# Kernel tuning notes

Hardware: AMD Instinct MI355X
Metric: run time of the kernel (lower is better)

The kernel has to match this reference:

```python
import math
import jax, jax.numpy as jnp
import numpy as np
from jax.scipy.special import xlogy

B, N, INP, E = 128, 16, 1024, 512
MU, CLF, PLCY = 512, 512, 512
M = N - 1          # merges (full tree)
T = N + M          # total tree tokens
L = N + M - 1      # logits matrix side
NOISE_STD, MASK_VAL = 0.01, -9e20
SFTMX_EPS, STD_EPS = 1e-20, 1e-20


def _mlp3(x, w1, b1, w2, b2, w3, b3):
    h = jax.nn.relu(x @ w1 + b1)
    h = jax.nn.relu(h @ w2 + b2)
    return h @ w3 + b3


def _lin(key, fi, fo):
    lim = math.sqrt(6.0 / (fi + fo))  # xavier uniform
    return (jax.random.uniform(key, (fi, fo), minval=-lim, maxval=lim, dtype=jnp.float32),
            jnp.full((fo,), 0.001, dtype=jnp.float32))


def setup_inputs():
    key = jax.random.key(0)
    ks = jax.random.split(key, 16)
    inp = {"x": jax.random.normal(ks[0], (B, N, INP), dtype=jnp.float32)}
    inp["lift_w"], inp["lift_b"] = _lin(ks[1], INP, E)
    inp["unlift_w"], inp["unlift_b"] = _lin(ks[2], E, INP)
    inp["enc_w1"], inp["enc_b1"] = _lin(ks[3], 2 * E, MU)
    inp["enc_w2"], inp["enc_b2"] = _lin(ks[4], MU, MU)
    inp["enc_w3"], inp["enc_b3"] = _lin(ks[5], MU, E)
    inp["dec_w1"], inp["dec_b1"] = _lin(ks[6], E, MU)
    inp["dec_w2"], inp["dec_b2"] = _lin(ks[7], MU, MU)
    inp["dec_w3"], inp["dec_b3"] = _lin(ks[8], MU, 2 * E)
    inp["clf_w1"], inp["clf_b1"] = _lin(ks[9], E, CLF)
    inp["clf_w2"], inp["clf_b2"] = _lin(ks[10], CLF, CLF)
    inp["clf_w3"], inp["clf_b3"] = _lin(ks[11], CLF, 2)
    inp["pol_w1"], inp["pol_b1"] = _lin(ks[12], 2 * E, PLCY)
    inp["pol_w2"], inp["pol_b2"] = _lin(ks[13], PLCY, PLCY)
    inp["pol_w3"], inp["pol_b3"] = _lin(ks[14], PLCY, 1)
    return inp


def _forward(x, lift_w, lift_b, unlift_w, unlift_b,
             enc_w1, enc_b1, enc_w2, enc_b2, enc_w3, enc_b3,
             dec_w1, dec_b1, dec_w2, dec_b2, dec_w3, dec_b3,
             clf_w1, clf_b1, clf_w2, clf_b2, clf_w3, clf_b3,
             pol_w1, pol_b1, pol_w2, pol_b2, pol_w3, pol_b3):
    sg = jax.lax.stop_gradient
    enc = lambda z: _mlp3(z, enc_w1, enc_b1, enc_w2, enc_b2, enc_w3, enc_b3)
    dec = lambda z: _mlp3(z, dec_w1, dec_b1, dec_w2, dec_b2, dec_w3, dec_b3)
    clf = lambda z: _mlp3(z, clf_w1, clf_b1, clf_w2, clf_b2, clf_w3, clf_b3)
    pol = lambda z: _mlp3(z, pol_w1, pol_b1, pol_w2, pol_b2, pol_w3, pol_b3)
    base = jax.random.key(42)
    b_idx = jnp.arange(B)

    # lift + noise
    u = x @ lift_w + lift_b
    u = u + NOISE_STD * jax.random.normal(jax.random.fold_in(base, 7), u.shape, u.dtype)

    logits_mtx = jnp.full((B, L, L), MASK_VAL, dtype=jnp.float32)
    # iter 0: score all ordered pairs (i,j), i != j, among input tokens (vectorized)
    ii, jj = np.where(~np.eye(N, dtype=bool))                 # P = N*(N-1) static pairs
    pair_x = jnp.concatenate([u[:, ii], u[:, jj]], axis=-1)   # [B,P,2E]
    logits_mtx = logits_mtx.at[:, ii, jj].set(pol(sg(pair_x))[..., 0])

    active = jnp.tile(jnp.arange(N, dtype=jnp.int32), (B, 1))
    step_losses = jnp.zeros(B, dtype=jnp.float32)
    entropies = jnp.zeros(B, dtype=jnp.float32)
    actions, log_probs, rewards = [], [], []

    for it in range(M):
        A = active.shape[1]  # = N - it (active-token count at entry)
        if it > 0:
            nt = N + it - 1                      # newest merged token (last in active)
            act = active[:, :-1]                 # [B, A-1] older active tokens
            u_act = u[b_idx[:, None], act]       # [B, A-1, E]
            u_nt = jnp.broadcast_to(u[:, nt][:, None, :], u_act.shape)
            lg_f = pol(sg(jnp.concatenate([u_nt, u_act], -1)))[..., 0]
            lg_b = pol(sg(jnp.concatenate([u_act, u_nt], -1)))[..., 0]
            logits_mtx = logits_mtx.at[b_idx[:, None], nt, act].set(lg_f)
            logits_mtx = logits_mtx.at[b_idx[:, None], act, nt].set(lg_b)

        flat = logits_mtx.reshape(B, L * L)      # temp == 1 for learned policy
        p = jax.nn.softmax(flat, axis=1)
        P2 = L * L
        p_adj = (p + SFTMX_EPS) / (1.0 + P2 * SFTMX_EPS)
        val_norm = SFTMX_EPS / (1.0 + P2 * SFTMX_EPS)
        opt_norm = A * (A - 1)
        nopt = P2 - opt_norm
        entrop = -(jnp.sum(xlogy(p_adj, p_adj), axis=1)
                   - nopt * (val_norm * math.log(val_norm))) / math.log(opt_norm)
        entropies = entropies + entrop

        # multinomial sample over flattened (masked) logits matrix
        sflat = jax.random.categorical(jax.random.fold_in(base, 100 + it), flat)
        s0, s1 = sflat // L, sflat % L
        sample = jnp.stack([s0, s1], axis=1)     # [B,2]
        actions.append(sample)
        log_probs.append(jnp.log(p[b_idx, sflat]))

        # mask out rows/cols of the merged tokens
        logits_mtx = logits_mtx.at[b_idx[:, None], sample, :].set(MASK_VAL)
        logits_mtx = logits_mtx.at[b_idx[:, None], :, sample].set(MASK_VAL)

        # remove the two sampled tokens from the active set (order-preserving)
        keep = (active != s0[:, None].astype(active.dtype)) & (active != s1[:, None].astype(active.dtype))
        order = jnp.argsort((~keep).astype(jnp.int32), axis=1, stable=True)
        active = jnp.take_along_axis(active, order[:, :A - 2], axis=1)

        pair = jnp.concatenate([u[b_idx, s0], u[b_idx, s1]], axis=1)  # [B,2E]
        true_s = sg(pair)
        pred_s = dec(enc(true_s))
        osl = jnp.sum((pred_s - true_s) ** 2, axis=1) / (2 * E)
        step_losses = step_losses + osl
        rewards.append(-sg(osl))

        # merge: encode pair (grad flows into u here) + noise, append to tree
        mg = enc(pair)
        mg = mg + NOISE_STD * jax.random.normal(jax.random.fold_in(base, 1000 + it), mg.shape, mg.dtype)
        u = jnp.concatenate([u, mg[:, None, :]], axis=1)
        active = jnp.concatenate([active, jnp.full((B, 1), N + it, dtype=active.dtype)], axis=1)

    actions = jnp.stack(actions, axis=1)    # [B,M,2]
    log_probs = jnp.stack(log_probs, axis=1)
    rewards = jnp.stack(rewards, axis=1)

    # top-down decode
    d = jnp.zeros_like(u)
    d = d.at[b_idx[:, None], active].set(u[b_idx[:, None], active])  # seed remaining active (root)
    clf_rows = []
    for it in range(M):
        tok = T - 1 - it
        mgd = d[:, tok]
        unmg = dec(mgd).reshape(B, 2, E)
        d = d.at[b_idx[:, None], actions[:, M - 1 - it]].set(unmg)
        clf_rows.append(clf(sg(mgd)))
    clf_pred = jnp.concatenate(
        [jnp.stack(clf_rows, axis=1), clf(sg(d[:, :N]))[:, ::-1, :]], axis=1)  # [B,M+N,2]
    clf_lbl = jnp.tile(jnp.concatenate(
        [jnp.ones(M, dtype=jnp.int32), jnp.zeros(N, dtype=jnp.int32)]), (B, 1))

    step_losses = step_losses / M
    entropies = entropies / M
    mvg = rewards.reshape(-1)  # B*M <= mvg_adv_sz, so moving buffer == current rewards
    rew_n = (rewards - mvg.mean()) / (jnp.std(mvg, ddof=1) + STD_EPS)
    reinf = jnp.sum(log_probs * rew_n, axis=1)
    recon = d[:, :N] @ unlift_w + unlift_b
    return recon, u, d, step_losses, entropies, clf_pred, clf_lbl, reinf


def reference(x, lift_w, lift_b, unlift_w, unlift_b,
              enc_w1, enc_b1, enc_w2, enc_b2, enc_w3, enc_b3,
              dec_w1, dec_b1, dec_w2, dec_b2, dec_w3, dec_b3,
              clf_w1, clf_b1, clf_w2, clf_b2, clf_w3, clf_b3,
              pol_w1, pol_b1, pol_w2, pol_b2, pol_w3, pol_b3):
    return _forward(x, lift_w, lift_b, unlift_w, unlift_b,
                    enc_w1, enc_b1, enc_w2, enc_b2, enc_w3, enc_b3,
                    dec_w1, dec_b1, dec_w2, dec_b2, dec_w3, dec_b3,
                    clf_w1, clf_b1, clf_w2, clf_b2, clf_w3, clf_b3,
                    pol_w1, pol_b1, pol_w2, pol_b2, pol_w3, pol_b3)
```

## Files before the change

kernel.cpp:

```cpp
#include <hip/hip_runtime.h>
#include <cstdint>
#include <cmath>

#define MASKV -9.0e20f

__host__ __device__ inline void tf2x32(uint32_t k0, uint32_t k1, uint32_t& x0, uint32_t& x1){
  uint32_t ks2 = k0 ^ k1 ^ 0x1BD11BDAu;
  x0 += k0; x1 += k1;
#define TFR(r) { x0 += x1; x1 = (x1<<(r))|(x1>>(32-(r))); x1 ^= x0; }
  TFR(13) TFR(15) TFR(26) TFR(6)
  x0 += k1;  x1 += ks2 + 1u;
  TFR(17) TFR(29) TFR(16) TFR(24)
  x0 += ks2; x1 += k0 + 2u;
  TFR(13) TFR(15) TFR(26) TFR(6)
  x0 += k0;  x1 += k1 + 3u;
  TFR(17) TFR(29) TFR(16) TFR(24)
  x0 += k1;  x1 += ks2 + 4u;
  TFR(13) TFR(15) TFR(26) TFR(6)
  x0 += ks2; x1 += k0 + 5u;
#undef TFR
}

__device__ inline uint32_t rbits32(uint32_t k0, uint32_t k1, uint32_t idx){
  uint32_t x0 = 0u, x1 = idx;
// ... 161 lines not shown
    float4 bb = *(const float4*)(b1 + ka);
    As[kq + 0][rA0] = fmaxf(p0.x + q0.x + bb.x, 0.f);
    As[kq + 1][rA0] = fmaxf(p0.y + q0.y + bb.y, 0.f);
    As[kq + 2][rA0] = fmaxf(p0.z + q0.z + bb.z, 0.f);
    As[kq + 3][rA0] = fmaxf(p0.w + q0.w + bb.w, 0.f);
    As[kq + 0][rA1] = fmaxf(p1.x + q1.x + bb.x, 0.f);
    As[kq + 1][rA1] = fmaxf(p1.y + q1.y + bb.y, 0.f);
    As[kq + 2][rA1] = fmaxf(p1.z + q1.z + bb.z, 0.f);
    As[kq + 3][rA1] = fmaxf(p1.w + q1.w + bb.w, 0.f);
    *(float4*)&Ws[wk0][wc0]     = *(const float4*)(W2 + (long)(k0 + wk0) * 512 + (c0 + wc0));
    *(float4*)&Ws[wk0 + 8][wc0] = *(const float4*)(W2 + (long)(k0 + wk0 + 8) * 512 + (c0 + wc0));
    __syncthreads();
#pragma unroll
    for (int kk = 0; kk < 16; kk++){
      float a0[8], w0[8];
      *(float4*)&a0[0] = *(const float4*)&As[kk][ty << 3];
      *(float4*)&a0[4] = *(const float4*)&As[kk][(ty << 3) + 4];
      *(float4*)&w0[0] = *(const float4*)&Ws[kk][tx << 3];
      *(float4*)&w0[4] = *(const float4*)&Ws[kk][(tx << 3) + 4];
#pragma unroll
      for (int i = 0; i < 8; i++)
#pragma unroll
        for (int j = 0; j < 8; j++)
          acc[i][j] = fmaf(a0[i], w0[j], acc[i][j]);
    }
    __syncthreads();
  }
  float bb[8], w3v[8];
  *(float4*)&bb[0] = *(const float4*)(b2 + c0 + (tx << 3));
  *(float4*)&bb[4] = *(const float4*)(b2 + c0 + (tx << 3) + 4);
  *(float4*)&w3v[0] = *(const float4*)(w3 + c0 + (tx << 3));
  *(float4*)&w3v[4] = *(const float4*)(w3 + c0 + (tx << 3) + 4);
#pragma unroll
  for (int i = 0; i < 8; i++){
    float p = 0.f;
#pragma unroll
    for (int j = 0; j < 8; j++)
      p = fmaf(fmaxf(acc[i][j] + bb[j], 0.f), w3v[j], p);
    for (int m = 1; m < 16; m <<= 1) p += __shfl_xor(p, m);
    if (tx == 0){
      int r = r0 + (ty << 3) + i;
      atomicAdd(logits + scat[r], p);
    }
  }
}

__global__ __launch_bounds__(256) void gemm64f_k(
    const float* __restrict__ Y,
    const long* __restrict__ atab,
    const float* __restrict__ b1,
    const float* __restrict__ W2, const float* __restrict__ b2,
    const float* __restrict__ w3,
    const int* __restrict__ scat, float* __restrict__ logits)
{
  __shared__ float As[16][64];
  __shared__ float Ws[16][64];
  int tid = threadIdx.x;
// ... 44 lines not shown
#pragma unroll
  for (int i = 0; i < 4; i++){
    float p = 0.f;
#pragma unroll
    for (int j = 0; j < 4; j++)
      p = fmaf(fmaxf(acc[i][j] + bb4[j], 0.f), w34[j], p);
    for (int m = 1; m < 16; m <<= 1) p += __shfl_xor(p, m);
    if (tx == 0){
      int r = r0 + (ty << 2) + i;
      atomicAdd(logits + scat[r], p);
    }
  }
}

__global__ __launch_bounds__(256) void rowdot_k(
    const float* __restrict__ A, int lda, const long* __restrict__ atab,
    const float* __restrict__ W, const float* __restrict__ bias,
    int K, int N, float* __restrict__ out, const int* __restrict__ scat,
    long c_base, int c_rdiv, long c_ostride, long c_istride)
{
  int wid = threadIdx.x >> 6, lane = threadIdx.x & 63;
  int r = blockIdx.x * 4 + wid;
  const float* a = atab ? (A + atab[r]) : (A + (long)r * lda);
  float s0 = 0.f, s1 = 0.f;
  for (int k = lane; k < K; k += 64){
    float x = a[k];
    s0 = fmaf(x, W[k * N], s0);
    if (N == 2) s1 = fmaf(x, W[k * N + 1], s1);
  }
  for (int off = 32; off > 0; off >>= 1){
    s0 += __shfl_down(s0, off);
    s1 += __shfl_down(s1, off);
  }
  if (lane == 0){
    if (scat){
      out[scat[r]] = s0 + bias[0];
    } else {
      long o = c_base + (long)(r / c_rdiv) * c_ostride + (long)(r % c_rdiv) * c_istride;
      out[o] = s0 + bias[0];
      if (N == 2) out[o + 1] = s1 + bias[1];
    }
  }
}

__global__ __launch_bounds__(256) void pairmv_k(
    const float* __restrict__ u, const long* __restrict__ tab_pair,
    const float* __restrict__ W, const float* __restrict__ bias,
    float* __restrict__ dst)
{
  __shared__ float s[1024];
  int b = blockIdx.y, tid = threadIdx.x;
  int c = blockIdx.x * 256 + tid;
  long t0 = tab_pair[b * 2], t1 = tab_pair[b * 2 + 1];
  s[tid]       = u[t0 + tid];
  s[tid + 256] = u[t0 + tid + 256];
  s[tid + 512] = u[t1 + tid];
  s[tid + 768] = u[t1 + tid + 256];
  __syncthreads();
  float a0 = 0.f, a1 = 0.f, a2 = 0.f, a3 = 0.f;
#pragma unroll 8
  for (int k = 0; k < 1024; k += 4){
    a0 = fmaf(s[k],     W[(long)k * 512 + c],       a0);
    a1 = fmaf(s[k + 1], W[(long)(k + 1) * 512 + c], a1);
    a2 = fmaf(s[k + 2], W[(long)(k + 2) * 512 + c], a2);
    a3 = fmaf(s[k + 3], W[(long)(k + 3) * 512 + c], a3);
  }
  float v = ((a0 + a1) + (a2 + a3)) + bias[c];
  dst[(long)b * 512 + c] = fmaxf(v, 0.f);
}

__global__ __launch_bounds__(256) void mvrelu_k(
    const float* __restrict__ src, long sstride,
    const float* __restrict__ W, const float* __restrict__ bias,
    float* __restrict__ dst)
{
  __shared__ float s[512];
  int b = blockIdx.y, tid = threadIdx.x;
  int c = blockIdx.x * 256 + tid;
  const float* sr = src + (long)b * sstride;
  s[tid] = sr[tid];
  s[tid + 256] = sr[tid + 256];
  __syncthreads();
  float a0 = 0.f, a1 = 0.f, a2 = 0.f, a3 = 0.f;
#pragma unroll 8
  for (int k = 0; k < 512; k += 4){
    a0 = fmaf(s[k],     W[(long)k * 512 + c],       a0);
    a1 = fmaf(s[k + 1], W[(long)(k + 1) * 512 + c], a1);
    a2 = fmaf(s[k + 2], W[(long)(k + 2) * 512 + c], a2);
    a3 = fmaf(s[k + 3], W[(long)(k + 3) * 512 + c], a3);
  }
  float v = ((a0 + a1) + (a2 + a3)) + bias[c];
  dst[(long)b * 512 + c] = fmaxf(v, 0.f);
}

__global__ __launch_bounds__(256) void lay3z_k(
    const float* __restrict__ src,
    const float* __restrict__ W, const float* __restrict__ bias,
    float* __restrict__ z_all, float* __restrict__ u,
    int it, uint32_t k0, uint32_t k1)
{
  __shared__ float s[512];
  int b = blockIdx.y, tid = threadIdx.x;
  int c = blockIdx.x * 256 + tid;
  const float* sr = src + (long)b * 512;
  s[tid] = sr[tid];
  s[tid + 256] = sr[tid + 256];
  __syncthreads();
  float a0 = 0.f, a1 = 0.f, a2 = 0.f, a3 = 0.f;
#pragma unroll 8
  for (int k = 0; k < 512; k += 4){
    a0 = fmaf(s[k],     W[(long)k * 512 + c],       a0);
    a1 = fmaf(s[k + 1], W[(long)(k + 1) * 512 + c], a1);
    a2 = fmaf(s[k + 2], W[(long)(k + 2) * 512 + c], a2);
    a3 = fmaf(s[k + 3], W[(long)(k + 3) * 512 + c], a3);
  }
  float v = ((a0 + a1) + (a2 + a3)) + bias[c];
  z_all[(long)it * 65536 + (long)b * 512 + c] = v;
  float nv = jax_normal(k0, k1, (uint32_t)(b * 512 + c));
  u[((long)(b * 31 + 16 + it)) * 512 + c] = v + 0.01f * nv;
}

__global__ __launch_bounds__(256) void yrow_k(
    const float* __restrict__ u, const float* __restrict__ W1cat,
    float* __restrict__ Y, int it)
{
  __shared__ float s[512];
  int b = blockIdx.y, tid = threadIdx.x;
  int c = blockIdx.x * 256 + tid;
  const float* sr = u + ((long)(b * 31 + 16 + it)) * 512;
  s[tid] = sr[tid];
  s[tid + 256] = sr[tid + 256];
  __syncthreads();
  float a0 = 0.f, a1 = 0.f, a2 = 0.f, a3 = 0.f;
#pragma unroll 8
  for (int k = 0; k < 512; k += 4){
    a0 = fmaf(s[k],     W1cat[(long)k * 1024 + c],       a0);
    a1 = fmaf(s[k + 1], W1cat[(long)(k + 1) * 1024 + c], a1);
    a2 = fmaf(s[k + 2], W1cat[(long)(k + 2) * 1024 + c], a2);
    a3 = fmaf(s[k + 3], W1cat[(long)(k + 3) * 1024 + c], a3);
  }
  Y[((long)(b * 31 + 16 + it)) * 1024 + c] = (a0 + a1) + (a2 + a3);
}

__global__ __launch_bounds__(256) void rev3_k(
    const float* __restrict__ src,
    const float* __restrict__ W, const float* __restrict__ bias,
    float* __restrict__ dmat, const int* __restrict__ actions, int it)
{
  __shared__ float s[512];
  int b = blockIdx.y, tid = threadIdx.x;
  int p = blockIdx.x * 256 + tid;
  const float* sr = src + (long)b * 512;
  s[tid] = sr[tid];
  s[tid + 256] = sr[tid + 256];
  __syncthreads();
  float a0 = 0.f, a1 = 0.f, a2 = 0.f, a3 = 0.f;
#pragma unroll 8
  for (int k = 0; k < 512; k += 4){
    a0 = fmaf(s[k],     W[(long)k * 1024 + p],       a0);
    a1 = fmaf(s[k + 1], W[(long)(k + 1) * 1024 + p], a1);
    a2 = fmaf(s[k + 2], W[(long)(k + 2) * 1024 + p], a2);
    a3 = fmaf(s[k + 3], W[(long)(k + 3) * 1024 + p], a3);
  }
  float v = ((a0 + a1) + (a2 + a3)) + bias[p];
  int fit = 14 - it;
  int s0 = actions[(b * 15 + fit) * 2];
  int s1 = actions[(b * 15 + fit) * 2 + 1];
  int node = (p < 512) ? s0 : s1;
  int ee = p & 511;
  dmat[((long)(b * 31 + node)) * 512 + ee] = v;
}

__global__ __launch_bounds__(256) void oslb_k(
    const float* __restrict__ pred, const float* __restrict__ u,
    const int* __restrict__ actions, float* __restrict__ sl, float* __restrict__ rew)
{
  int r = blockIdx.x, tid = threadIdx.x;
  int it = r >> 7, b = r & 127;
  int s0 = actions[(b * 15 + it) * 2];
  int s1 = actions[(b * 15 + it) * 2 + 1];
  const float* t0 = u + ((long)(b * 31 + s0)) * 512;
  const float* t1 = u + ((long)(b * 31 + s1)) * 512;
  const float* p = pred + (long)r * 1024;
  float s = 0.f;
  for (int k = tid; k < 512; k += 256){
    float d0 = p[k] - t0[k];       s = fmaf(d0, d0, s);
    float d1 = p[k + 512] - t1[k]; s = fmaf(d1, d1, s);
  }
  __shared__ float red[256];
  red[tid] = s; __syncthreads();
  for (int st = 128; st > 0; st >>= 1){ if (tid < st) red[tid] += red[tid + st]; __syncthreads(); }
  if (tid == 0){
    float osl = red[0] / 1024.0f;
    atomicAdd(sl + b, osl);
    rew[b * 15 + it] = -osl;
  }
}

__global__ __launch_bounds__(256) void init_k(float* __restrict__ dmat, float* __restrict__ lbl,
    float* __restrict__ logits, float* __restrict__ sl, float* __restrict__ ent,
    int* __restrict__ active, float* __restrict__ zb,
    float* __restrict__ W1cat, const float* __restrict__ pol_w1, const float* __restrict__ pol_b3,
    long* __restrict__ tab_init, int* __restrict__ scat_init, long* __restrict__ tab_tok16,
    long* __restrict__ tab_mgd)
{
  long i = (long)blockIdx.x * 256 + threadIdx.x;
  if (i < 2031616L) dmat[i] = 0.f;
  if (i < 524288L){
    int k = (int)(i >> 10), n = (int)(i & 1023);
    W1cat[i] = (n < 512) ? pol_w1[(long)k * 512 + n] : pol_w1[(long)(k + 512) * 512 + (n - 512)];
  }
  if (i < 115200L){
    int rem = (int)(i % 900);
    int rr = rem / 30, cc = rem % 30;
    logits[i] = (rr < 16 && cc < 16 && rr != cc) ? pol_b3[0] : MASKV;
  }
  if (i < 30720L){
    int r = (int)i;
    int pk = r >> 7, b = r & 127;
    int ii2 = pk / 15, jr = pk % 15;
    int jj2 = jr + (jr >= ii2 ? 1 : 0);
    tab_init[r * 2]     = ((long)(b * 31 + ii2)) * 1024;
    tab_init[r * 2 + 1] = ((long)(b * 31 + jj2)) * 1024 + 512;
    scat_init[r] = b * 900 + ii2 * 30 + jj2;
  }
  if (i < 3968L)  lbl[i] = ((i % 31) < 15) ? 1.0f : 0.0f;
  if (i < 2048L){
    active[i] = (int)(i & 15);
    tab_tok16[i] = ((long)((i >> 4) * 31 + (i & 15))) * 512;
  }
  if (i < 1920L){
    int it = (int)(i >> 7), b = (int)(i & 127);
    tab_mgd[i] = ((long)(b * 31 + 30 - it)) * 512;
  }
  if (i < 1024L)  zb[i] = 0.f;
  if (i < 128L){ sl[i] = 0.f; ent[i] = 0.f; }
}

__global__ __launch_bounds__(256) void noise_u_k(float* __restrict__ u, uint32_t k0, uint32_t k1){
  uint32_t e = blockIdx.x * 256u + threadIdx.x;
  uint32_t b = e >> 13, rem = e & 8191u, n = rem >> 9, ee = rem & 511u;
  float nr = jax_normal(k0, k1, e);
  long off = ((long)(b * 31u + n)) * 512 + ee;
  u[off] += 0.01f * nr;
}

__global__ __launch_bounds__(256) void build_d_k(float* __restrict__ dmat, const float* __restrict__ u){
  int e = blockIdx.x * 256 + threadIdx.x;
  int b = e >> 9, ee = e & 511;
  long off = ((long)(b * 31 + 30)) * 512 + ee;
  dmat[off] = u[off];
}

__global__ __launch_bounds__(256) void sample_k(float* __restrict__ logits, int* __restrict__ active,
    int* __restrict__ actions, float* __restrict__ lp, float* __restrict__ ent,
    int it, int A, uint32_t k0, uint32_t k1, float log_opt,
    long* __restrict__ tab_loop, int* __restrict__ scat_loop, long* __restrict__ tab_pair,
    const float* __restrict__ pol_b3)
{
  int b = blockIdx.x, tid = threadIdx.x;
  float* Lg = logits + (long)b * 900;
  __shared__ float red[256];
  __shared__ int redi[256];
  __shared__ int ss0, ss1;

  float v = -3.4e38f;
  for (int j = tid; j < 900; j += 256) v = fmaxf(v, Lg[j]);
  red[tid] = v; __syncthreads();
  for (int s = 128; s > 0; s >>= 1){ if (tid < s) red[tid] = fmaxf(red[tid], red[tid + s]); __syncthreads(); }
  float m = red[0]; __syncthreads();

  float acc = 0.f;
  for (int j = tid; j < 900; j += 256) acc += expf(Lg[j] - m);
  red[tid] = acc; __syncthreads();
  for (int s = 128; s > 0; s >>= 1){ if (tid < s) red[tid] += red[tid + s]; __syncthreads(); }
  float ssum = red[0]; __syncthreads();

  float es = 0.f;
  for (int j = tid; j < 900; j += 256){
    float l = Lg[j];
    if (l > MASKV){
      float p = expf(l - m) / ssum;
      float pa = p + 1e-20f;
      es += pa * logf(pa);
    }
  }
  red[tid] = es; __syncthreads();
  for (int s = 128; s > 0; s >>= 1){ if (tid < s) red[tid] += red[tid + s]; __syncthreads(); }
  if (tid == 0) ent[b] += -(red[0]) / log_opt;
  __syncthreads();

  float bv = -3.4e38f; int bi = 0;
  for (int j = tid; j < 900; j += 256){
    float g = jax_gumbel(k0, k1, (uint32_t)(b * 900 + j));
    float val = Lg[j] + g;
    if (val > bv){ bv = val; bi = j; }
  }
  red[tid] = bv; redi[tid] = bi; __syncthreads();
  for (int s = 128; s > 0; s >>= 1){
    if (tid < s){
      float o = red[tid + s]; int oi = redi[tid + s];
      if (o > red[tid] || (o == red[tid] && oi < redi[tid])){ red[tid] = o; redi[tid] = oi; }
    }
    __syncthreads();
  }
  if (tid == 0){
    int sf = redi[0];
    int s0 = sf / 30, s1 = sf % 30;
    ss0 = s0; ss1 = s1;
    actions[(b * 15 + it) * 2] = s0;
    actions[(b * 15 + it) * 2 + 1] = s1;
    lp[b * 15 + it] = Lg[sf] - m - logf(ssum);
    tab_pair[b * 2]     = ((long)(b * 31 + s0)) * 512;
    tab_pair[b * 2 + 1] = ((long)(b * 31 + s1)) * 512;
  }
  __syncthreads();
  int s0 = ss0, s1 = ss1;
  if (tid < 30){
    Lg[s0 * 30 + tid] = MASKV;
    Lg[s1 * 30 + tid] = MASKV;
    Lg[tid * 30 + s0] = MASKV;
    Lg[tid * 30 + s1] = MASKV;
  }
  if (tid == 0){
    float b3v = pol_b3[0];
    int buf[16]; int c = 0;
    for (int k = 0; k < A; k++){
      int a = active[b * 16 + k];
      if (a != s0 && a != s1) buf[c++] = a;
// ... 6 lines not shown
      int q = buf[j];
      int r1 = j * 128 + b;
      tab_loop[r1 * 2]     = ((long)(b * 31 + nt2)) * 1024;
      tab_loop[r1 * 2 + 1] = ((long)(b * 31 + q)) * 1024 + 512;
      int sc1 = b * 900 + nt2 * 30 + q;
      scat_loop[r1] = sc1;
      logits[sc1] = b3v;
      int r2 = (na2 + j) * 128 + b;
      tab_loop[r2 * 2]     = ((long)(b * 31 + q)) * 1024;
      tab_loop[r2 * 2 + 1] = ((long)(b * 31 + nt2)) * 1024 + 512;
      int sc2 = b * 900 + q * 30 + nt2;
      scat_loop[r2] = sc2;
      logits[sc2] = b3v;
    }
  }
}

__global__ __launch_bounds__(256) void finalize_k(const float* __restrict__ rew,
    const float* __restrict__ lp, const float* __restrict__ sl, const float* __restrict__ ent,
    float* __restrict__ out_sl, float* __restrict__ out_ent, float* __restrict__ out_reinf)
{
  __shared__ float red[256];
  int tid = threadIdx.x;
  float s = 0.f;
  for (int i = tid; i < 1920; i += 256) s += rew[i];
  red[tid] = s; __syncthreads();
  for (int st = 128; st > 0; st >>= 1){ if (tid < st) red[tid] += red[tid + st]; __syncthreads(); }
  float mean = red[0] / 1920.0f; __syncthreads();
  float v = 0.f;
  for (int i = tid; i < 1920; i += 256){ float x = rew[i] - mean; v = fmaf(x, x, v); }
// ... 55 lines not shown
  const long LBL_OFF   = 6168576;
  const long REINF_OFF = 6172544;
  float* recon = out;
  float* u     = out + U_OFF;
  float* dmat  = out + D_OFF;

  char* wsb = (char*)d_ws;
  size_t wo = 0;
  auto alloc = [&](size_t bytes) -> void* {
    void* p = (void*)(wsb + wo);
    wo = (wo + bytes + 255) & ~(size_t)255;
    return p;
  };
  float* logits    = (float*)alloc(115200 * 4);
  float* Y         = (float*)alloc((size_t)3968 * 1024 * 4);
  float* pbuf      = Y;
  float* W1cat     = (float*)alloc((size_t)524288 * 4);
  float* zb        = (float*)alloc(1024 * 4);
  float* h1        = (float*)alloc((size_t)2048 * 512 * 4);
  float* h2        = (float*)alloc((size_t)2048 * 512 * 4);
  float* z_all     = (float*)alloc((size_t)15 * 65536 * 4);
  float* sl        = (float*)alloc(128 * 4);
  float* ent       = (float*)alloc(128 * 4);
  float* lp        = (float*)alloc(1920 * 4);
  float* rew       = (float*)alloc(1920 * 4);
  int*   active    = (int*)alloc(2048 * 4);
  int*   actions   = (int*)alloc(3840 * 4);
  long*  tab_init  = (long*)alloc((size_t)30720 * 2 * 8);
  int*   scat_init = (int*)alloc(30720 * 4);
  long*  tab_loop  = (long*)alloc((size_t)3584 * 2 * 8);
  int*   scat_loop = (int*)alloc(3584 * 4);
  long*  tab_pair  = (long*)alloc(256 * 8);
  long*  tab_tok16 = (long*)alloc(2048 * 8);
  long*  tab_mgd   = (long*)alloc(1920 * 8);
  (void)ws_size; (void)in_sizes; (void)n_in; (void)out_size;

  uint32_t k7a, k7b, ck0[15], ck1[15], mk0[15], mk1[15];
  { uint32_t a = 0, b = 7; tf2x32(0u, 42u, a, b); k7a = a; k7b = b; }
  for (int it = 0; it < 15; it++){
    { uint32_t a = 0, b = (uint32_t)(100 + it); tf2x32(0u, 42u, a, b); ck0[it] = a; ck1[it] = b; }
    { uint32_t a = 0, b = (uint32_t)(1000 + it); tf2x32(0u, 42u, a, b); mk0[it] = a; mk1[it] = b; }
  }

  auto gemm = [&](int act, const float* A, int lda, const long* atab, int anblk,
                  const float* W, const float* bs, float* C, int rows, int K, int Nn,
                  long cb, int crd, long cos, long cis){
    dim3 g(Nn / 64, rows / 64);
// ... 11 lines not shown
  gemm(0, u, 0, tab_tok16, 1, W1cat, zb, Y, 2048, 512, 1024, 0, 16, 31744, 1024);

  { dim3 g(4, 240);
    gemm128f_k<<<g, 256, 0, stream>>>(Y, tab_init, pol_b1, pol_w2, pol_b2, pol_w3,
                                      scat_init, logits); }

  for (int it = 0; it < 15; it++){
    int A = 16 - it;
    if (it > 0){
      int rows = 256 * (15 - it);
      dim3 g(8, rows / 64);
      gemm64f_k<<<g, 256, 0, stream>>>(Y, tab_loop, pol_b1, pol_w2, pol_b2, pol_w3,
                                       scat_loop, logits);
    }
    float log_opt = (float)log((double)(A * (A - 1)));
    sample_k<<<128, 256, 0, stream>>>(logits, active, actions, lp, ent, it, A,
                                      ck0[it], ck1[it], log_opt,
                                      tab_loop, scat_loop, tab_pair, pol_b3);
    { dim3 g(2, 128);
      pairmv_k<<<g, 256, 0, stream>>>(u, tab_pair, enc_w1, enc_b1, h1); }
    { dim3 g(2, 128);
      mvrelu_k<<<g, 256, 0, stream>>>(h1, 512, enc_w2, enc_b2, h2); }
    { dim3 g(2, 128);
      lay3z_k<<<g, 256, 0, stream>>>(h2, enc_w3, enc_b3, z_all, u, it, mk0[it], mk1[it]); }
    if (it < 14){
      dim3 g(4, 128);
      yrow_k<<<g, 256, 0, stream>>>(u, W1cat, Y, it);
    }
  }

  gemm(1, z_all, 512, nullptr, 0, dec_w1, dec_b1, h1, 1920, 512, 512, 0, 1, 512, 0);
  gemm(1, h1, 512, nullptr, 0, dec_w2, dec_b2, h2, 1920, 512, 512, 0, 1, 512, 0);
  gemm(0, h2, 512, nullptr, 0, dec_w3, dec_b3, pbuf, 1920, 512, 1024, 0, 1, 1024, 0);
  oslb_k<<<1920, 256, 0, stream>>>(pbuf, u, actions, sl, rew);

  build_d_k<<<256, 256, 0, stream>>>(dmat, u);

  for (int it = 0; it < 15; it++){
    int tok = 30 - it;
    { dim3 g(2, 128);
      mvrelu_k<<<g, 256, 0, stream>>>(dmat + (long)tok * 512, 15872, dec_w1, dec_b1, h1); }
    { dim3 g(2, 128);
      mvrelu_k<<<g, 256, 0, stream>>>(h1, 512, dec_w2, dec_b2, h2); }
    { dim3 g(4, 128);
      rev3_k<<<g, 256, 0, stream>>>(h2, dec_w3, dec_b3, dmat, actions, it); }
  }

  gemm(1, dmat, 0, tab_mgd, 1, clf_w1, clf_b1, h1, 1920, 512, 512, 0, 1, 512, 0);
  gemm(1, h1, 512, nullptr, 0, clf_w2, clf_b2, h2, 1920, 512, 512, 0, 1, 512, 0);
  rowdot_k<<<480, 256, 0, stream>>>(h2, 512, nullptr, clf_w3, clf_b3, 512, 2,
                                    out, nullptr, CLF_OFF, 128, 2, 62);

  gemm(1, dmat, 0, tab_tok16, 1, clf_w1, clf_b1, h1, 2048, 512, 512, 0, 1, 512, 0);
  gemm(1, h1, 512, nullptr, 0, clf_w2, clf_b2, h2, 2048, 512, 512, 0, 1, 512, 0);
  rowdot_k<<<512, 256, 0, stream>>>(h2, 512, nullptr, clf_w3, clf_b3, 512, 2,
                                    out, nullptr, CLF_OFF + 60, 16, 62, -2);

  gemm(0, dmat, 0, tab_tok16, 1, unlift_w, unlift_b, recon, 2048, 512, 1024,
       0, 16, 16384, 1024);

  finalize_k<<<1, 256, 0, stream>>>(rew, lp, sl, ent,
                                    out + SL_OFF, out + ENT_OFF, out + REINF_OFF);
}
```

Measured before the change: 2.621 ms.

## Fuse sampling and encoder MLP chain into one per-batch kernel; fuse decoder reverse loop

Replaces the per-iteration sequence of sample, pair-matvec, two matvec-relu layers and the Y-row update with a single 1024-thread kernel per batch row. That kernel does sampling, the three encoder layers via a shared-memory split-K helper, noise injection and the Y row. The reverse decoder loop becomes one fused kernel per step, and build_d is folded into its first iteration. The 128-wide GEMM also switches its thread-to-row/column mapping to strided halves, which should reduce LDS bank conflicts. Far fewer launches per step are traded for only 128 blocks doing weight-streaming matvecs, which may limit memory parallelism.

```diff
diff --git a/kernel.cpp b/kernel.cpp
--- a/kernel.cpp
+++ b/kernel.cpp
@@ -199,10 +199,10 @@
 #pragma unroll
     for (int kk = 0; kk < 16; kk++){
       float a0[8], w0[8];
-      *(float4*)&a0[0] = *(const float4*)&As[kk][ty << 3];
-      *(float4*)&a0[4] = *(const float4*)&As[kk][(ty << 3) + 4];
-      *(float4*)&w0[0] = *(const float4*)&Ws[kk][tx << 3];
-      *(float4*)&w0[4] = *(const float4*)&Ws[kk][(tx << 3) + 4];
+      *(float4*)&a0[0] = *(const float4*)&As[kk][ty << 2];
+      *(float4*)&a0[4] = *(const float4*)&As[kk][(ty << 2) + 64];
+      *(float4*)&w0[0] = *(const float4*)&Ws[kk][tx << 2];
+      *(float4*)&w0[4] = *(const float4*)&Ws[kk][(tx << 2) + 64];
 #pragma unroll
       for (int i = 0; i < 8; i++)
 #pragma unroll
@@ -212,10 +212,10 @@
     __syncthreads();
   }
   float bb[8], w3v[8];
-  *(float4*)&bb[0] = *(const float4*)(b2 + c0 + (tx << 3));
-  *(float4*)&bb[4] = *(const float4*)(b2 + c0 + (tx << 3) + 4);
-  *(float4*)&w3v[0] = *(const float4*)(w3 + c0 + (tx << 3));
-  *(float4*)&w3v[4] = *(const float4*)(w3 + c0 + (tx << 3) + 4);
+  *(float4*)&bb[0]  = *(const float4*)(b2 + c0 + (tx << 2));
+  *(float4*)&bb[4]  = *(const float4*)(b2 + c0 + (tx << 2) + 64);
+  *(float4*)&w3v[0] = *(const float4*)(w3 + c0 + (tx << 2));
+  *(float4*)&w3v[4] = *(const float4*)(w3 + c0 + (tx << 2) + 64);
 #pragma unroll
   for (int i = 0; i < 8; i++){
     float p = 0.f;
@@ -224,8 +224,8 @@
       p = fmaf(fmaxf(acc[i][j] + bb[j], 0.f), w3v[j], p);
     for (int m = 1; m < 16; m <<= 1) p += __shfl_xor(p, m);
     if (tx == 0){
-      int r = r0 + (ty << 3) + i;
-      atomicAdd(logits + scat[r], p);
+      int rr = (i < 4) ? ((ty << 2) + i) : (64 + (ty << 2) + (i - 4));
+      atomicAdd(logits + scat[r0 + rr], p);
     }
   }
 }
@@ -300,290 +300,96 @@
 }
 
 __global__ __launch_bounds__(256) void rowdot_k(
-    const float* __restrict__ A, int lda, const long* __restrict__ atab,
+    const float* __restrict__ A, int lda,
     const float* __restrict__ W, const float* __restrict__ bias,
-    int K, int N, float* __restrict__ out, const int* __restrict__ scat,
+    int K, float* __restrict__ out,
     long c_base, int c_rdiv, long c_ostride, long c_istride)
 {
   int wid = threadIdx.x >> 6, lane = threadIdx.x & 63;
   int r = blockIdx.x * 4 + wid;
-  const float* a = atab ? (A + atab[r]) : (A + (long)r * lda);
+  const float* a = A + (long)r * lda;
   float s0 = 0.f, s1 = 0.f;
   for (int k = lane; k < K; k += 64){
     float x = a[k];
-    s0 = fmaf(x, W[k * N], s0);
-    if (N == 2) s1 = fmaf(x, W[k * N + 1], s1);
+    s0 = fmaf(x, W[k * 2], s0);
+    s1 = fmaf(x, W[k * 2 + 1], s1);
   }
   for (int off = 32; off > 0; off >>= 1){
     s0 += __shfl_down(s0, off);
     s1 += __shfl_down(s1, off);
   }
   if (lane == 0){
-    if (scat){
-      out[scat[r]] = s0 + bias[0];
-    } else {
-      long o = c_base + (long)(r / c_rdiv) * c_ostride + (long)(r % c_rdiv) * c_istride;
-      out[o] = s0 + bias[0];
-      if (N == 2) out[o + 1] = s1 + bias[1];
-    }
-  }
-}
-
-__global__ __launch_bounds__(256) void pairmv_k(
-    const float* __restrict__ u, const long* __restrict__ tab_pair,
-    const float* __restrict__ W, const float* __restrict__ bias,
-    float* __restrict__ dst)
-{
-  __shared__ float s[1024];
-  int b = blockIdx.y, tid = threadIdx.x;
-  int c = blockIdx.x * 256 + tid;
-  long t0 = tab_pair[b * 2], t1 = tab_pair[b * 2 + 1];
-  s[tid]       = u[t0 + tid];
-  s[tid + 256] = u[t0 + tid + 256];
-  s[tid + 512] = u[t1 + tid];
-  s[tid + 768] = u[t1 + tid + 256];
-  __syncthreads();
+    long o = c_base + (long)(r / c_rdiv) * c_ostride + (long)(r % c_rdiv) * c_istride;
+    out[o] = s0 + bias[0];
+    out[o + 1] = s1 + bias[1];
+  }
+}
+
+__device__ inline void mlayer(const float* __restrict__ W, const float* __restrict__ bias,
+    const float* src, float* dst, float (*ps)[512], int Khalf, int relu, int tid)
+{
+  int c = tid & 511, ks = tid >> 9;
+  int kb = ks * Khalf;
   float a0 = 0.f, a1 = 0.f, a2 = 0.f, a3 = 0.f;
 #pragma unroll 8
-  for (int k = 0; k < 1024; k += 4){
-    a0 = fmaf(s[k],     W[(long)k * 512 + c],       a0);
-    a1 = fmaf(s[k + 1], W[(long)(k + 1) * 512 + c], a1);
-    a2 = fmaf(s[k + 2], W[(long)(k + 2) * 512 + c], a2);
-    a3 = fmaf(s[k + 3], W[(long)(k + 3) * 512 + c], a3);
-  }
-  float v = ((a0 + a1) + (a2 + a3)) + bias[c];
-  dst[(long)b * 512 + c] = fmaxf(v, 0.f);
-}
-
-__global__ __launch_bounds__(256) void mvrelu_k(
-    const float* __restrict__ src, long sstride,
-    const float* __restrict__ W, const float* __restrict__ bias,
-    float* __restrict__ dst)
-{
-  __shared__ float s[512];
-  int b = blockIdx.y, tid = threadIdx.x;
-  int c = blockIdx.x * 256 + tid;
-  const float* sr = src + (long)b * sstride;
-  s[tid] = sr[tid];
-  s[tid + 256] = sr[tid + 256];
+  for (int k = kb; k < kb + Khalf; k += 4){
+    a0 = fmaf(src[k],     W[(long)k * 512 + c],       a0);
+    a1 = fmaf(src[k + 1], W[(long)(k + 1) * 512 + c], a1);
+    a2 = fmaf(src[k + 2], W[(long)(k + 2) * 512 + c], a2);
+    a3 = fmaf(src[k + 3], W[(long)(k + 3) * 512 + c], a3);
+  }
+  ps[ks][c] = (a0 + a1) + (a2 + a3);
   __syncthreads();
-  float a0 = 0.f, a1 = 0.f, a2 = 0.f, a3 = 0.f;
-#pragma unroll 8
-  for (int k = 0; k < 512; k += 4){
-    a0 = fmaf(s[k],     W[(long)k * 512 + c],       a0);
-    a1 = fmaf(s[k + 1], W[(long)(k + 1) * 512 + c], a1);
-    a2 = fmaf(s[k + 2], W[(long)(k + 2) * 512 + c], a2);
-    a3 = fmaf(s[k + 3], W[(long)(k + 3) * 512 + c], a3);
-  }
-  float v = ((a0 + a1) + (a2 + a3)) + bias[c];
-  dst[(long)b * 512 + c] = fmaxf(v, 0.f);
-}
-
-__global__ __launch_bounds__(256) void lay3z_k(
-    const float* __restrict__ src,
-    const float* __restrict__ W, const float* __restrict__ bias,
-    float* __restrict__ z_all, float* __restrict__ u,
-    int it, uint32_t k0, uint32_t k1)
-{
-  __shared__ float s[512];
-  int b = blockIdx.y, tid = threadIdx.x;
-  int c = blockIdx.x * 256 + tid;
-  const float* sr = src + (long)b * 512;
-  s[tid] = sr[tid];
-  s[tid + 256] = sr[tid + 256];
+  if (tid < 512){
+    float v = ps[0][tid] + ps[1][tid] + bias[tid];
+    dst[tid] = relu ? fmaxf(v, 0.f) : v;
+  }
   __syncthreads();
-  float a0 = 0.f, a1 = 0.f, a2 = 0.f, a3 = 0.f;
-#pragma unroll 8
-  for (int k = 0; k < 512; k += 4){
-    a0 = fmaf(s[k],     W[(long)k * 512 + c],       a0);
-    a1 = fmaf(s[k + 1], W[(long)(k + 1) * 512 + c], a1);
-    a2 = fmaf(s[k + 2], W[(long)(k + 2) * 512 + c], a2);
-    a3 = fmaf(s[k + 3], W[(long)(k + 3) * 512 + c], a3);
-  }
-  float v = ((a0 + a1) + (a2 + a3)) + bias[c];
-  z_all[(long)it * 65536 + (long)b * 512 + c] = v;
-  float nv = jax_normal(k0, k1, (uint32_t)(b * 512 + c));
-  u[((long)(b * 31 + 16 + it)) * 512 + c] = v + 0.01f * nv;
-}
-
-__global__ __launch_bounds__(256) void yrow_k(
-    const float* __restrict__ u, const float* __restrict__ W1cat,
-    float* __restrict__ Y, int it)
-{
-  __shared__ float s[512];
-  int b = blockIdx.y, tid = threadIdx.x;
-  int c = blockIdx.x * 256 + tid;
-  const float* sr = u + ((long)(b * 31 + 16 + it)) * 512;
-  s[tid] = sr[tid];
-  s[tid + 256] = sr[tid + 256];
-  __syncthreads();
-  float a0 = 0.f, a1 = 0.f, a2 = 0.f, a3 = 0.f;
-#pragma unroll 8
-  for (int k = 0; k < 512; k += 4){
-    a0 = fmaf(s[k],     W1cat[(long)k * 1024 + c],       a0);
-    a1 = fmaf(s[k + 1], W1cat[(long)(k + 1) * 1024 + c], a1);
-    a2 = fmaf(s[k + 2], W1cat[(long)(k + 2) * 1024 + c], a2);
-    a3 = fmaf(s[k + 3], W1cat[(long)(k + 3) * 1024 + c], a3);
-  }
-  Y[((long)(b * 31 + 16 + it)) * 1024 + c] = (a0 + a1) + (a2 + a3);
-}
-
-__global__ __launch_bounds__(256) void rev3_k(
-    const float* __restrict__ src,
-    const float* __restrict__ W, const float* __restrict__ bias,
-    float* __restrict__ dmat, const int* __restrict__ actions, int it)
-{
-  __shared__ float s[512];
-  int b = blockIdx.y, tid = threadIdx.x;
-  int p = blockIdx.x * 256 + tid;
-  const float* sr = src + (long)b * 512;
-  s[tid] = sr[tid];
-  s[tid + 256] = sr[tid + 256];
-  __syncthreads();
-  float a0 = 0.f, a1 = 0.f, a2 = 0.f, a3 = 0.f;
-#pragma unroll 8
-  for (int k = 0; k < 512; k += 4){
-    a0 = fmaf(s[k],     W[(long)k * 1024 + p],       a0);
-    a1 = fmaf(s[k + 1], W[(long)(k + 1) * 1024 + p], a1);
-    a2 = fmaf(s[k + 2], W[(long)(k + 2) * 1024 + p], a2);
-    a3 = fmaf(s[k + 3], W[(long)(k + 3) * 1024 + p], a3);
-  }
-  float v = ((a0 + a1) + (a2 + a3)) + bias[p];
-  int fit = 14 - it;
-  int s0 = actions[(b * 15 + fit) * 2];
-  int s1 = actions[(b * 15 + fit) * 2 + 1];
-  int node = (p < 512) ? s0 : s1;
-  int ee = p & 511;
-  dmat[((long)(b * 31 + node)) * 512 + ee] = v;
-}
-
-__global__ __launch_bounds__(256) void oslb_k(
-    const float* __restrict__ pred, const float* __restrict__ u,
-    const int* __restrict__ actions, float* __restrict__ sl, float* __restrict__ rew)
-{
-  int r = blockIdx.x, tid = threadIdx.x;
-  int it = r >> 7, b = r & 127;
-  int s0 = actions[(b * 15 + it) * 2];
-  int s1 = actions[(b * 15 + it) * 2 + 1];
-  const float* t0 = u + ((long)(b * 31 + s0)) * 512;
-  const float* t1 = u + ((long)(b * 31 + s1)) * 512;
-  const float* p = pred + (long)r * 1024;
-  float s = 0.f;
-  for (int k = tid; k < 512; k += 256){
-    float d0 = p[k] - t0[k];       s = fmaf(d0, d0, s);
-    float d1 = p[k + 512] - t1[k]; s = fmaf(d1, d1, s);
-  }
-  __shared__ float red[256];
-  red[tid] = s; __syncthreads();
-  for (int st = 128; st > 0; st >>= 1){ if (tid < st) red[tid] += red[tid + st]; __syncthreads(); }
-  if (tid == 0){
-    float osl = red[0] / 1024.0f;
-    atomicAdd(sl + b, osl);
-    rew[b * 15 + it] = -osl;
-  }
-}
-
-__global__ __launch_bounds__(256) void init_k(float* __restrict__ dmat, float* __restrict__ lbl,
-    float* __restrict__ logits, float* __restrict__ sl, float* __restrict__ ent,
-    int* __restrict__ active, float* __restrict__ zb,
-    float* __restrict__ W1cat, const float* __restrict__ pol_w1, const float* __restrict__ pol_b3,
-    long* __restrict__ tab_init, int* __restrict__ scat_init, long* __restrict__ tab_tok16,
-    long* __restrict__ tab_mgd)
-{
-  long i = (long)blockIdx.x * 256 + threadIdx.x;
-  if (i < 2031616L) dmat[i] = 0.f;
-  if (i < 524288L){
-    int k = (int)(i >> 10), n = (int)(i & 1023);
-    W1cat[i] = (n < 512) ? pol_w1[(long)k * 512 + n] : pol_w1[(long)(k + 512) * 512 + (n - 512)];
-  }
-  if (i < 115200L){
-    int rem = (int)(i % 900);
-    int rr = rem / 30, cc = rem % 30;
-    logits[i] = (rr < 16 && cc < 16 && rr != cc) ? pol_b3[0] : MASKV;
-  }
-  if (i < 30720L){
-    int r = (int)i;
-    int pk = r >> 7, b = r & 127;
-    int ii2 = pk / 15, jr = pk % 15;
-    int jj2 = jr + (jr >= ii2 ? 1 : 0);
-    tab_init[r * 2]     = ((long)(b * 31 + ii2)) * 1024;
-    tab_init[r * 2 + 1] = ((long)(b * 31 + jj2)) * 1024 + 512;
-    scat_init[r] = b * 900 + ii2 * 30 + jj2;
-  }
-  if (i < 3968L)  lbl[i] = ((i % 31) < 15) ? 1.0f : 0.0f;
-  if (i < 2048L){
-    active[i] = (int)(i & 15);
-    tab_tok16[i] = ((long)((i >> 4) * 31 + (i & 15))) * 512;
-  }
-  if (i < 1920L){
-    int it = (int)(i >> 7), b = (int)(i & 127);
-    tab_mgd[i] = ((long)(b * 31 + 30 - it)) * 512;
-  }
-  if (i < 1024L)  zb[i] = 0.f;
-  if (i < 128L){ sl[i] = 0.f; ent[i] = 0.f; }
-}
-
-__global__ __launch_bounds__(256) void noise_u_k(float* __restrict__ u, uint32_t k0, uint32_t k1){
-  uint32_t e = blockIdx.x * 256u + threadIdx.x;
-  uint32_t b = e >> 13, rem = e & 8191u, n = rem >> 9, ee = rem & 511u;
-  float nr = jax_normal(k0, k1, e);
-  long off = ((long)(b * 31u + n)) * 512 + ee;
-  u[off] += 0.01f * nr;
-}
-
-__global__ __launch_bounds__(256) void build_d_k(float* __restrict__ dmat, const float* __restrict__ u){
-  int e = blockIdx.x * 256 + threadIdx.x;
-  int b = e >> 9, ee = e & 511;
-  long off = ((long)(b * 31 + 30)) * 512 + ee;
-  dmat[off] = u[off];
-}
-
-__global__ __launch_bounds__(256) void sample_k(float* __restrict__ logits, int* __restrict__ active,
+}
+
+__global__ __launch_bounds__(1024) void sampenc_k(
+    float* __restrict__ logits, int* __restrict__ active,
     int* __restrict__ actions, float* __restrict__ lp, float* __restrict__ ent,
-    int it, int A, uint32_t k0, uint32_t k1, float log_opt,
-    long* __restrict__ tab_loop, int* __restrict__ scat_loop, long* __restrict__ tab_pair,
-    const float* __restrict__ pol_b3)
+    float* __restrict__ u, float* __restrict__ Y, float* __restrict__ z_all,
+    const float* __restrict__ ew1, const float* __restrict__ eb1,
+    const float* __restrict__ ew2, const float* __restrict__ eb2,
+    const float* __restrict__ ew3, const float* __restrict__ eb3,
+    const float* __restrict__ W1cat,
+    long* __restrict__ tab_loop, int* __restrict__ scat_loop,
+    const float* __restrict__ pol_b3,
+    int it, int A, uint32_t ck0, uint32_t ck1, uint32_t mk0, uint32_t mk1, float log_opt)
 {
   int b = blockIdx.x, tid = threadIdx.x;
   float* Lg = logits + (long)b * 900;
-  __shared__ float red[256];
-  __shared__ int redi[256];
+  __shared__ float red[1024];
+  __shared__ int redi[1024];
+  __shared__ float sIn[1024];
+  __shared__ float ps[2][512];
+  __shared__ float hA[512], hB[512];
   __shared__ int ss0, ss1;
 
-  float v = -3.4e38f;
-  for (int j = tid; j < 900; j += 256) v = fmaxf(v, Lg[j]);
-  red[tid] = v; __syncthreads();
-  for (int s = 128; s > 0; s >>= 1){ if (tid < s) red[tid] = fmaxf(red[tid], red[tid + s]); __syncthreads(); }
+  float l = (tid < 900) ? Lg[tid] : -3.4e38f;
+  red[tid] = l; __syncthreads();
+  for (int s = 512; s > 0; s >>= 1){ if (tid < s) red[tid] = fmaxf(red[tid], red[tid + s]); __syncthreads(); }
   float m = red[0]; __syncthreads();
-
-  float acc = 0.f;
-  for (int j = tid; j < 900; j += 256) acc += expf(Lg[j] - m);
-  red[tid] = acc; __syncthreads();
-  for (int s = 128; s > 0; s >>= 1){ if (tid < s) red[tid] += red[tid + s]; __syncthreads(); }
+  float e = (tid < 900) ? expf(l - m) : 0.f;
+  red[tid] = e; __syncthreads();
+  for (int s = 512; s > 0; s >>= 1){ if (tid < s) red[tid] += red[tid + s]; __syncthreads(); }
   float ssum = red[0]; __syncthreads();
-
   float es = 0.f;
-  for (int j = tid; j < 900; j += 256){
-    float l = Lg[j];
-    if (l > MASKV){
-      float p = expf(l - m) / ssum;
-      float pa = p + 1e-20f;
-      es += pa * logf(pa);
-    }
+  if (tid < 900 && l > MASKV){
+    float p = e / ssum;
+    float pa = p + 1e-20f;
+    es = pa * logf(pa);
   }
   red[tid] = es; __syncthreads();
-  for (int s = 128; s > 0; s >>= 1){ if (tid < s) red[tid] += red[tid + s]; __syncthreads(); }
+  for (int s = 512; s > 0; s >>= 1){ if (tid < s) red[tid] += red[tid + s]; __syncthreads(); }
   if (tid == 0) ent[b] += -(red[0]) / log_opt;
   __syncthreads();
 
-  float bv = -3.4e38f; int bi = 0;
-  for (int j = tid; j < 900; j += 256){
-    float g = jax_gumbel(k0, k1, (uint32_t)(b * 900 + j));
-    float val = Lg[j] + g;
-    if (val > bv){ bv = val; bi = j; }
-  }
-  red[tid] = bv; redi[tid] = bi; __syncthreads();
-  for (int s = 128; s > 0; s >>= 1){
+  float g = (tid < 900) ? (l + jax_gumbel(ck0, ck1, (uint32_t)(b * 900 + tid))) : -3.4e38f;
+  red[tid] = g; redi[tid] = tid; __syncthreads();
+  for (int s = 512; s > 0; s >>= 1){
     if (tid < s){
       float o = red[tid + s]; int oi = redi[tid + s];
       if (o > red[tid] || (o == red[tid] && oi < redi[tid])){ red[tid] = o; redi[tid] = oi; }
@@ -597,8 +403,6 @@
     actions[(b * 15 + it) * 2] = s0;
     actions[(b * 15 + it) * 2 + 1] = s1;
     lp[b * 15 + it] = Lg[sf] - m - logf(ssum);
-    tab_pair[b * 2]     = ((long)(b * 31 + s0)) * 512;
-    tab_pair[b * 2 + 1] = ((long)(b * 31 + s1)) * 512;
   }
   __syncthreads();
   int s0 = ss0, s1 = ss1;
@@ -635,6 +439,143 @@
       logits[sc2] = b3v;
     }
   }
+
+  sIn[tid] = (tid < 512) ? u[((long)(b * 31 + s0)) * 512 + tid]
+                         : u[((long)(b * 31 + s1)) * 512 + (tid - 512)];
+  __syncthreads();
+  mlayer(ew1, eb1, sIn, hA, ps, 512, 1, tid);
+  mlayer(ew2, eb2, hA, hB, ps, 256, 1, tid);
+  mlayer(ew3, eb3, hB, hA, ps, 256, 0, tid);
+  if (tid < 512){
+    float z = hA[tid];
+    z_all[(long)it * 65536 + (long)b * 512 + tid] = z;
+    float uv = z + 0.01f * jax_normal(mk0, mk1, (uint32_t)(b * 512 + tid));
+    u[((long)(b * 31 + 16 + it)) * 512 + tid] = uv;
+    hB[tid] = uv;
+  }
+  __syncthreads();
+  if (it < 14){
+    float a0 = 0.f, a1 = 0.f, a2 = 0.f, a3 = 0.f;
+#pragma unroll 8
+    for (int k = 0; k < 512; k += 4){
+      a0 = fmaf(hB[k],     W1cat[(long)k * 1024 + tid],       a0);
+      a1 = fmaf(hB[k + 1], W1cat[(long)(k + 1) * 1024 + tid], a1);
+      a2 = fmaf(hB[k + 2], W1cat[(long)(k + 2) * 1024 + tid], a2);
+      a3 = fmaf(hB[k + 3], W1cat[(long)(k + 3) * 1024 + tid], a3);
+    }
+    Y[((long)(b * 31 + 16 + it)) * 1024 + tid] = (a0 + a1) + (a2 + a3);
+  }
+}
+
+__global__ __launch_bounds__(1024) void rev_k(
+    float* __restrict__ dmat, const float* __restrict__ u,
+    const int* __restrict__ actions,
+    const float* __restrict__ dw1, const float* __restrict__ db1,
+    const float* __restrict__ dw2, const float* __restrict__ db2,
+    const float* __restrict__ dw3, const float* __restrict__ db3,
+    int it)
+{
+  __shared__ float sA[512], sB[512];
+  __shared__ float ps[2][512];
+  int b = blockIdx.x, tid = threadIdx.x;
+  int tok = 30 - it, fit = 14 - it;
+  if (tid < 512){
+    long off = ((long)(b * 31 + tok)) * 512 + tid;
+    float v;
+    if (it == 0){ v = u[off]; dmat[off] = v; }
+    else v = dmat[off];
+    sA[tid] = v;
+  }
+  __syncthreads();
+  mlayer(dw1, db1, sA, sB, ps, 256, 1, tid);
+  mlayer(dw2, db2, sB, sA, ps, 256, 1, tid);
+  float a0 = 0.f, a1 = 0.f, a2 = 0.f, a3 = 0.f;
+#pragma unroll 8
+  for (int k = 0; k < 512; k += 4){
+    a0 = fmaf(sA[k],     dw3[(long)k * 1024 + tid],       a0);
+    a1 = fmaf(sA[k + 1], dw3[(long)(k + 1) * 1024 + tid], a1);
+    a2 = fmaf(sA[k + 2], dw3[(long)(k + 2) * 1024 + tid], a2);
+    a3 = fmaf(sA[k + 3], dw3[(long)(k + 3) * 1024 + tid], a3);
+  }
+  float v = ((a0 + a1) + (a2 + a3)) + db3[tid];
+  int s0 = actions[(b * 15 + fit) * 2];
+  int s1 = actions[(b * 15 + fit) * 2 + 1];
+  int node = (tid < 512) ? s0 : s1;
+  dmat[((long)(b * 31 + node)) * 512 + (tid & 511)] = v;
+}
+
+__global__ __launch_bounds__(256) void oslb_k(
+    const float* __restrict__ pred, const float* __restrict__ u,
+    const int* __restrict__ actions, float* __restrict__ sl, float* __restrict__ rew)
+{
+  int r = blockIdx.x, tid = threadIdx.x;
+  int it = r >> 7, b = r & 127;
+  int s0 = actions[(b * 15 + it) * 2];
+  int s1 = actions[(b * 15 + it) * 2 + 1];
+  const float* t0 = u + ((long)(b * 31 + s0)) * 512;
+  const float* t1 = u + ((long)(b * 31 + s1)) * 512;
+  const float* p = pred + (long)r * 1024;
+  float s = 0.f;
+  for (int k = tid; k < 512; k += 256){
+    float d0 = p[k] - t0[k];       s = fmaf(d0, d0, s);
+    float d1 = p[k + 512] - t1[k]; s = fmaf(d1, d1, s);
+  }
+  __shared__ float red[256];
+  red[tid] = s; __syncthreads();
+  for (int st = 128; st > 0; st >>= 1){ if (tid < st) red[tid] += red[tid + st]; __syncthreads(); }
+  if (tid == 0){
+    float osl = red[0] / 1024.0f;
+    atomicAdd(sl + b, osl);
+    rew[b * 15 + it] = -osl;
+  }
+}
+
+__global__ __launch_bounds__(256) void init_k(float* __restrict__ dmat, float* __restrict__ lbl,
+    float* __restrict__ logits, float* __restrict__ sl, float* __restrict__ ent,
+    int* __restrict__ active, float* __restrict__ zb,
+    float* __restrict__ W1cat, const float* __restrict__ pol_w1, const float* __restrict__ pol_b3,
+    long* __restrict__ tab_init, int* __restrict__ scat_init, long* __restrict__ tab_tok16,
+    long* __restrict__ tab_mgd)
+{
+  long i = (long)blockIdx.x * 256 + threadIdx.x;
+  if (i < 2031616L) dmat[i] = 0.f;
+  if (i < 524288L){
+    int k = (int)(i >> 10), n = (int)(i & 1023);
+    W1cat[i] = (n < 512) ? pol_w1[(long)k * 512 + n] : pol_w1[(long)(k + 512) * 512 + (n - 512)];
+  }
+  if (i < 115200L){
+    int rem = (int)(i % 900);
+    int rr = rem / 30, cc = rem % 30;
+    logits[i] = (rr < 16 && cc < 16 && rr != cc) ? pol_b3[0] : MASKV;
+  }
+  if (i < 30720L){
+    int r = (int)i;
+    int pk = r >> 7, b = r & 127;
+    int ii2 = pk / 15, jr = pk % 15;
+    int jj2 = jr + (jr >= ii2 ? 1 : 0);
+    tab_init[r * 2]     = ((long)(b * 31 + ii2)) * 1024;
+    tab_init[r * 2 + 1] = ((long)(b * 31 + jj2)) * 1024 + 512;
+    scat_init[r] = b * 900 + ii2 * 30 + jj2;
+  }
+  if (i < 3968L)  lbl[i] = ((i % 31) < 15) ? 1.0f : 0.0f;
+  if (i < 2048L){
+    active[i] = (int)(i & 15);
+    tab_tok16[i] = ((long)((i >> 4) * 31 + (i & 15))) * 512;
+  }
+  if (i < 1920L){
+    int it = (int)(i >> 7), b = (int)(i & 127);
+    tab_mgd[i] = ((long)(b * 31 + 30 - it)) * 512;
+  }
+  if (i < 1024L)  zb[i] = 0.f;
+  if (i < 128L){ sl[i] = 0.f; ent[i] = 0.f; }
+}
+
+__global__ __launch_bounds__(256) void noise_u_k(float* __restrict__ u, uint32_t k0, uint32_t k1){
+  uint32_t e = blockIdx.x * 256u + threadIdx.x;
+  uint32_t b = e >> 13, rem = e & 8191u, n = rem >> 9, ee = rem & 511u;
+  float nr = jax_normal(k0, k1, e);
+  long off = ((long)(b * 31u + n)) * 512 + ee;
+  u[off] += 0.01f * nr;
 }
 
 __global__ __launch_bounds__(256) void finalize_k(const float* __restrict__ rew,
@@ -720,11 +661,11 @@
   };
   float* logits    = (float*)alloc(115200 * 4);
   float* Y         = (float*)alloc((size_t)3968 * 1024 * 4);
-  float* pbuf      = Y;
+  float* h2ov      = Y;
+  float* pbuf      = Y + 2031616;
   float* W1cat     = (float*)alloc((size_t)524288 * 4);
   float* zb        = (float*)alloc(1024 * 4);
   float* h1        = (float*)alloc((size_t)2048 * 512 * 4);
-  float* h2        = (float*)alloc((size_t)2048 * 512 * 4);
   float* z_all     = (float*)alloc((size_t)15 * 65536 * 4);
   float* sl        = (float*)alloc(128 * 4);
   float* ent       = (float*)alloc(128 * 4);
@@ -736,7 +677,6 @@
   int*   scat_init = (int*)alloc(30720 * 4);
   long*  tab_loop  = (long*)alloc((size_t)3584 * 2 * 8);
   int*   scat_loop = (int*)alloc(3584 * 4);
-  long*  tab_pair  = (long*)alloc(256 * 8);
   long*  tab_tok16 = (long*)alloc(2048 * 8);
   long*  tab_mgd   = (long*)alloc(1920 * 8);
   (void)ws_size; (void)in_sizes; (void)n_in; (void)out_size;
@@ -778,47 +718,32 @@
                                        scat_loop, logits);
     }
     float log_opt = (float)log((double)(A * (A - 1)));
-    sample_k<<<128, 256, 0, stream>>>(logits, active, actions, lp, ent, it, A,
-                                      ck0[it], ck1[it], log_opt,
-                                      tab_loop, scat_loop, tab_pair, pol_b3);
-    { dim3 g(2, 128);
-      pairmv_k<<<g, 256, 0, stream>>>(u, tab_pair, enc_w1, enc_b1, h1); }
-    { dim3 g(2, 128);
-      mvrelu_k<<<g, 256, 0, stream>>>(h1, 512, enc_w2, enc_b2, h2); }
-    { dim3 g(2, 128);
-      lay3z_k<<<g, 256, 0, stream>>>(h2, enc_w3, enc_b3, z_all, u, it, mk0[it], mk1[it]); }
-    if (it < 14){
-      dim3 g(4, 128);
-      yrow_k<<<g, 256, 0, stream>>>(u, W1cat, Y, it);
-    }
+    sampenc_k<<<128, 1024, 0, stream>>>(logits, active, actions, lp, ent,
+                                        u, Y, z_all,
+                                        enc_w1, enc_b1, enc_w2, enc_b2, enc_w3, enc_b3,
+                                        W1cat, tab_loop, scat_loop, pol_b3,
+                                        it, A, ck0[it], ck1[it], mk0[it], mk1[it], log_opt);
   }
 
   gemm(1, z_all, 512, nullptr, 0, dec_w1, dec_b1, h1, 1920, 512, 512, 0, 1, 512, 0);
-  gemm(1, h1, 512, nullptr, 0, dec_w2, dec_b2, h2, 1920, 512, 512, 0, 1, 512, 0);
-  gemm(0, h2, 512, nullptr, 0, dec_w3, dec_b3, pbuf, 1920, 512, 1024, 0, 1, 1024, 0);
+  gemm(1, h1, 512, nullptr, 0, dec_w2, dec_b2, h2ov, 1920, 512, 512, 0, 1, 512, 0);
+  gemm(0, h2ov, 512, nullptr, 0, dec_w3, dec_b3, pbuf, 1920, 512, 1024, 0, 1, 1024, 0);
   oslb_k<<<1920, 256, 0, stream>>>(pbuf, u, actions, sl, rew);
 
-  build_d_k<<<256, 256, 0, stream>>>(dmat, u);
-
   for (int it = 0; it < 15; it++){
-    int tok = 30 - it;
-    { dim3 g(2, 128);
-      mvrelu_k<<<g, 256, 0, stream>>>(dmat + (long)tok * 512, 15872, dec_w1, dec_b1, h1); }
-    { dim3 g(2, 128);
-      mvrelu_k<<<g, 256, 0, stream>>>(h1, 512, dec_w2, dec_b2, h2); }
-    { dim3 g(4, 128);
-      rev3_k<<<g, 256, 0, stream>>>(h2, dec_w3, dec_b3, dmat, actions, it); }
+    rev_k<<<128, 1024, 0, stream>>>(dmat, u, actions,
+                                    dec_w1, dec_b1, dec_w2, dec_b2, dec_w3, dec_b3, it);
   }
 
   gemm(1, dmat, 0, tab_mgd, 1, clf_w1, clf_b1, h1, 1920, 512, 512, 0, 1, 512, 0);
-  gemm(1, h1, 512, nullptr, 0, clf_w2, clf_b2, h2, 1920, 512, 512, 0, 1, 512, 0);
-  rowdot_k<<<480, 256, 0, stream>>>(h2, 512, nullptr, clf_w3, clf_b3, 512, 2,
-                                    out, nullptr, CLF_OFF, 128, 2, 62);
+  gemm(1, h1, 512, nullptr, 0, clf_w2, clf_b2, h2ov, 1920, 512, 512, 0, 1, 512, 0);
+  rowdot_k<<<480, 256, 0, stream>>>(h2ov, 512, clf_w3, clf_b3, 512,
+                                    out, CLF_OFF, 128, 2, 62);
 
   gemm(1, dmat, 0, tab_tok16, 1, clf_w1, clf_b1, h1, 2048, 512, 512, 0, 1, 512, 0);
-  gemm(1, h1, 512, nullptr, 0, clf_w2, clf_b2, h2, 2048, 512, 512, 0, 1, 512, 0);
-  rowdot_k<<<512, 256, 0, stream>>>(h2, 512, nullptr, clf_w3, clf_b3, 512, 2,
-                                    out, nullptr, CLF_OFF + 60, 16, 62, -2);
+  gemm(1, h1, 512, nullptr, 0, clf_w2, clf_b2, h2ov, 2048, 512, 512, 0, 1, 512, 0);
+  rowdot_k<<<512, 256, 0, stream>>>(h2ov, 512, clf_w3, clf_b3, 512,
+                                    out, CLF_OFF + 60, 16, 62, -2);
 
   gemm(0, dmat, 0, tab_tok16, 1, unlift_w, unlift_b, recon, 2048, 512, 1024,
        0, 16, 16384, 1024);
```

New measurement: 2.846 ms. 8.6% more time.
